# Kernel tuning notes

Hardware: AMD Instinct MI355X
Metric: run time of the kernel (lower is better)

## Reference

```python
import jax, jax.numpy as jnp
import numpy as np

# unit constants from Converter._set_unit (astropy values, precomputed):
# unit_nu_f_nu = Lsun / (4*pi*(10 pc)^2) in erg/s/cm^2
UNIT_NU_F_NU = 3.1995e-07
# unit_f_nu = unit_nu_f_nu / (c / angstrom) in Jy
UNIT_F_NU = 1.0673e-02


def setup_inputs() -> dict:
    key = jax.random.key(0)
    k1, k2 = jax.random.split(key)
    B, F, L = 8192, 128, 8192
    # strictly increasing wavelength grid in Angstrom
    lam = 100.0 + 6.0 * (jnp.arange(L, dtype=jnp.float32) + 1.0)
    # positive fluxes so log10 is defined
    l_target = jax.random.uniform(k1, (B, L), dtype=jnp.float32) + 0.1
    # filter transmissions (already unit-normalized in __init__); keep positive
    trans_filter = 1e-3 * (jax.random.uniform(k2, (F, L), dtype=jnp.float32) + 0.01)
    return {"l_target": l_target, "trans_filter": trans_filter, "lam": lam, "return_ph": 1}


def reference(l_target, trans_filter, lam, return_ph):
    if return_ph:
        # trapz(y, x) == sum_l y[l] * w[l] with trapezoid weights w from lam.
        dx = jnp.diff(lam)  # [L-1]
        w = jnp.zeros_like(lam).at[:-1].add(0.5 * dx).at[1:].add(0.5 * dx)  # [L]
        # fuse weights into the filter matrix -> single GEMM, no [B,F,L] intermediate
        wt = trans_filter * w[None, :]  # [F, L]
        flux = jnp.einsum('bl,fl->bf', l_target, wt)  # [B, F]
        return -2.5 * jnp.log10(flux)
    else:
        return l_target * lam[None, :] * UNIT_F_NU
```

## Files before the change

kernel.cpp:

```cpp
#include <hip/hip_runtime.h>
#include <hip/hip_bf16.h>
#include <cstdint>

#define B_ROWS 8192
#define F_FILT 128
#define L_LEN  8192
#define SPLITK 4
#define KCHUNK (L_LEN / SPLITK)
#define STEPS  (KCHUNK / 32)
#define WM     16
#define WAVES  2
#define BM     (WM * WAVES)
#define MBLK   (B_ROWS / BM)

typedef __attribute__((ext_vector_type(4))) float f32x4;
typedef __attribute__((ext_vector_type(8))) short bf16x8;

__device__ __forceinline__ short f2bf(float f) {
  union { float f; unsigned u; } v; v.f = f;
  unsigned u = v.u + 0x7FFFu + ((v.u >> 16) & 1u);
  return (short)(u >> 16);
}

__device__ __forceinline__ bf16x8 cvt8(f32x4 x, f32x4 y) {
  union { unsigned u[4]; bf16x8 v; } r;
  asm("v_cvt_pk_bf16_f32 %0, %1, %2" : "=v"(r.u[0]) : "v"(x[0]), "v"(x[1]));
  asm("v_cvt_pk_bf16_f32 %0, %1, %2" : "=v"(r.u[1]) : "v"(x[2]), "v"(x[3]));
  asm("v_cvt_pk_bf16_f32 %0, %1, %2" : "=v"(r.u[2]) : "v"(y[0]), "v"(y[1]));
  asm("v_cvt_pk_bf16_f32 %0, %1, %2" : "=v"(r.u[3]) : "v"(y[2]), "v"(y[3]));
  return r.v;
}

__global__ void build_wt(const float* __restrict__ trans,
                         const float* __restrict__ lam,
                         ushort* __restrict__ bp) {
  int o = blockIdx.x * blockDim.x + threadIdx.x;
  int lane = o & 63, j = (o >> 6) & 7, gs = o >> 9;
  int f = j * 16 + (lane & 15);
  int k = gs * 32 + (lane >> 4) * 8;
  bf16x8 h;
#pragma unroll
  for (int i = 0; i < 8; ++i) {
    int l = k + i;
    float lo = (l > 0)         ? lam[l - 1] : lam[0];
    float hi = (l < L_LEN - 1) ? lam[l + 1] : lam[L_LEN - 1];
    h[i] = f2bf(trans[(size_t)f * L_LEN + l] * (0.5f * (hi - lo)));
  }
  *(bf16x8*)(bp + (size_t)o * 8) = h;
}

__global__ __launch_bounds__(128, 4)
void gemm_splitk(const float* __restrict__ A,
                 const ushort* __restrict__ BP,
                 float* __restrict__ P ) {
  const int lane = threadIdx.x & 63;
  const int wave = threadIdx.x >> 6;
  const int rl = lane & 15;
  const int kg = lane >> 4;
  const int m0 = blockIdx.x * BM + wave * WM;
  const int s  = blockIdx.y;
  const int k0 = s * KCHUNK;

  const uint32_t aoff = (uint32_t)(m0 + rl) * L_LEN + (uint32_t)k0 + (uint32_t)kg * 8;
  const uint32_t boff = ((uint32_t)(k0 / 32) * 512u + (uint32_t)lane) * 8u;

  f32x4 acc[8] = {};

  f32x4 an0 = *(const f32x4*)(A + aoff);
  f32x4 an1 = *(const f32x4*)(A + aoff + 4);
  f32x4 am0 = *(const f32x4*)(A + aoff + 32);
  f32x4 am1 = *(const f32x4*)(A + aoff + 36);

#pragma unroll
  for (int st = 0; st < STEPS; ++st) {
    f32x4 ac0 = an0, ac1 = an1;
    an0 = am0; an1 = am1;
    if (st + 2 < STEPS) {
      am0 = *(const f32x4*)(A + aoff + (st + 2) * 32);
      am1 = *(const f32x4*)(A + aoff + (st + 2) * 32 + 4);
    }
    bf16x8 af = cvt8(ac0, ac1);
    const ushort* pbs0 = BP + boff + (size_t)st * 4096;
    const ushort* pbs1 = pbs0 + 2048;
#pragma unroll
    for (int j = 0; j < 4; ++j) {
      bf16x8 b = *(const bf16x8*)(pbs0 + j * 512);
      acc[j] = __builtin_amdgcn_mfma_f32_16x16x32_bf16(af, b, acc[j], 0, 0, 0);
    }
#pragma unroll
    for (int j = 0; j < 4; ++j) {
      bf16x8 b = *(const bf16x8*)(pbs1 + j * 512);
      acc[4 + j] = __builtin_amdgcn_mfma_f32_16x16x32_bf16(af, b, acc[4 + j], 0, 0, 0);
    }
  }

  float* po = P + ((size_t)s * B_ROWS + m0) * F_FILT;
#pragma unroll
  for (int r = 0; r < 4; ++r) {
    const int row = kg * 4 + r;
#pragma unroll
    for (int j = 0; j < 8; ++j)
      po[(size_t)row * F_FILT + j * 16 + rl] = acc[j][r];
  }
}

__global__ void finish(const float* __restrict__ P, float* __restrict__ out) {
  int t = blockIdx.x * blockDim.x + threadIdx.x;
  f32x4 s = {};
#pragma unroll
  for (int i = 0; i < SPLITK; ++i) {
    f32x4 p = *(const f32x4*)(P + (size_t)i * ((size_t)B_ROWS * F_FILT) + (size_t)t * 4);
    s[0] += p[0]; s[1] += p[1]; s[2] += p[2]; s[3] += p[3];
  }
  f32x4 o;
  o[0] = -2.5f * log10f(s[0]);
  o[1] = -2.5f * log10f(s[1]);
  o[2] = -2.5f * log10f(s[2]);
  o[3] = -2.5f * log10f(s[3]);
  *(f32x4*)(out + (size_t)t * 4) = o;
}

extern "C" void kernel_launch(void* const* d_in, const int* in_sizes, int n_in,
                              void* d_out, int out_size, void* d_ws, size_t ws_size,
                              hipStream_t stream) {
  const float* A    = (const float*)d_in[0];
  const float* T    = (const float*)d_in[1];
  const float* lam  = (const float*)d_in[2];

  ushort* bp = (ushort*)d_ws;
  float*  P  = (float*)((char*)d_ws + (size_t)F_FILT * L_LEN * sizeof(ushort));
  float*  out = (float*)d_out;

  build_wt<<<(F_FILT * L_LEN / 8) / 256, 256, 0, stream>>>(T, lam, bp);
  gemm_splitk<<<dim3(MBLK, SPLITK), 128, 0, stream>>>(A, bp, P);
  finish<<<(B_ROWS * F_FILT / 4) / 256, 256, 0, stream>>>(P, out);
}
```

Before: 506.8 us.

## Stage filter tiles in LDS shared by eight waves, raise split-K to 16

Measured after the change: 412.6 us. -18.6%, faster.

```diff
diff --git a/kernel.cpp b/kernel.cpp
--- a/kernel.cpp
+++ b/kernel.cpp
@@ -5,12 +5,11 @@
 #define B_ROWS 8192
 #define F_FILT 128
 #define L_LEN  8192
-#define SPLITK 4
+#define SPLITK 16
 #define KCHUNK (L_LEN / SPLITK)
-#define STEPS  (KCHUNK / 32)
-#define WM     16
-#define WAVES  2
-#define BM     (WM * WAVES)
+#define PH_G   8
+#define WAVES  8
+#define BM     128
 #define MBLK   (B_ROWS / BM)
 
 typedef __attribute__((ext_vector_type(4))) float f32x4;
@@ -49,20 +48,22 @@
   *(bf16x8*)(bp + (size_t)o * 8) = h;
 }
 
-__global__ __launch_bounds__(128, 4)
+__global__ __launch_bounds__(512, 2)
 void gemm_splitk(const float* __restrict__ A,
                  const ushort* __restrict__ BP,
                  float* __restrict__ P ) {
-  const int lane = threadIdx.x & 63;
-  const int wave = threadIdx.x >> 6;
+  __shared__ ushort smem[PH_G * 8 * 64 * 8];
+  const int tid  = threadIdx.x;
+  const int lane = tid & 63;
+  const int wave = tid >> 6;
   const int rl = lane & 15;
   const int kg = lane >> 4;
-  const int m0 = blockIdx.x * BM + wave * WM;
+  const int m0 = blockIdx.x * BM + wave * 16;
   const int s  = blockIdx.y;
   const int k0 = s * KCHUNK;
 
   const uint32_t aoff = (uint32_t)(m0 + rl) * L_LEN + (uint32_t)k0 + (uint32_t)kg * 8;
-  const uint32_t boff = ((uint32_t)(k0 / 32) * 512u + (uint32_t)lane) * 8u;
+  const ushort* bpc = BP + (size_t)s * 65536;
 
   f32x4 acc[8] = {};
 
@@ -72,26 +73,33 @@
   f32x4 am1 = *(const f32x4*)(A + aoff + 36);
 
 #pragma unroll
-  for (int st = 0; st < STEPS; ++st) {
-    f32x4 ac0 = an0, ac1 = an1;
-    an0 = am0; an1 = am1;
-    if (st + 2 < STEPS) {
-      am0 = *(const f32x4*)(A + aoff + (st + 2) * 32);
-      am1 = *(const f32x4*)(A + aoff + (st + 2) * 32 + 4);
+  for (int p = 0; p < 2; ++p) {
+    {
+      const f32x4* src = (const f32x4*)(bpc + (size_t)p * 32768);
+      f32x4* dst = (f32x4*)smem;
+#pragma unroll
+      for (int it = 0; it < 8; ++it)
+        dst[it * 512 + tid] = src[it * 512 + tid];
     }
-    bf16x8 af = cvt8(ac0, ac1);
-    const ushort* pbs0 = BP + boff + (size_t)st * 4096;
-    const ushort* pbs1 = pbs0 + 2048;
+    __syncthreads();
 #pragma unroll
-    for (int j = 0; j < 4; ++j) {
-      bf16x8 b = *(const bf16x8*)(pbs0 + j * 512);
-      acc[j] = __builtin_amdgcn_mfma_f32_16x16x32_bf16(af, b, acc[j], 0, 0, 0);
+    for (int st = 0; st < PH_G; ++st) {
+      const int ss = p * PH_G + st;
+      f32x4 ac0 = an0, ac1 = an1;
+      an0 = am0; an1 = am1;
+      if (ss + 2 < 16) {
+        am0 = *(const f32x4*)(A + aoff + (ss + 2) * 32);
+        am1 = *(const f32x4*)(A + aoff + (ss + 2) * 32 + 4);
+      }
+      bf16x8 af = cvt8(ac0, ac1);
+      const ushort* bsrc = smem + st * 4096 + lane * 8;
+#pragma unroll
+      for (int j = 0; j < 8; ++j) {
+        bf16x8 b = *(const bf16x8*)(bsrc + j * 512);
+        acc[j] = __builtin_amdgcn_mfma_f32_16x16x32_bf16(af, b, acc[j], 0, 0, 0);
+      }
     }
-#pragma unroll
-    for (int j = 0; j < 4; ++j) {
-      bf16x8 b = *(const bf16x8*)(pbs1 + j * 512);
-      acc[4 + j] = __builtin_amdgcn_mfma_f32_16x16x32_bf16(af, b, acc[4 + j], 0, 0, 0);
-    }
+    __syncthreads();
   }
 
   float* po = P + ((size_t)s * B_ROWS + m0) * F_FILT;
@@ -132,6 +140,6 @@
   float*  out = (float*)d_out;
 
   build_wt<<<(F_FILT * L_LEN / 8) / 256, 256, 0, stream>>>(T, lam, bp);
-  gemm_splitk<<<dim3(MBLK, SPLITK), 128, 0, stream>>>(A, bp, P);
+  gemm_splitk<<<dim3(MBLK, SPLITK), 512, 0, stream>>>(A, bp, P);
   finish<<<(B_ROWS * F_FILT / 4) / 256, 256, 0, stream>>>(P, out);
 }
```
